# Kernel tuning notes

Measured on AMD Instinct MI355X. Metric: run time of the kernel, lower is better.

## Reference

```python
import jax, jax.numpy as jnp
import numpy as np

DIM_IN, DIM_OUT, DIM_CTX = 128, 256, 259
B, N, S_CTX = 32, 2048, 1
BN_EPS = 1e-5


def setup_inputs() -> dict:
    key = jax.random.key(0)
    ks = jax.random.split(key, 12)
    s = 0.02
    return {
        "ctx": jax.random.normal(ks[0], (B, S_CTX, DIM_CTX), jnp.float32),
        "x": jax.random.normal(ks[1], (B, N, DIM_IN), jnp.float32),
        "W_layer": jax.random.normal(ks[2], (DIM_OUT, DIM_IN), jnp.float32) * s,
        "b_layer": jax.random.normal(ks[3], (DIM_OUT,), jnp.float32) * s,
        "W_hbias": jax.random.normal(ks[4], (DIM_OUT, DIM_CTX), jnp.float32) * s,
        "W_gate": jax.random.normal(ks[5], (DIM_OUT, DIM_CTX), jnp.float32) * s,
        "b_gate": jax.random.normal(ks[6], (DIM_OUT,), jnp.float32) * s,
        "W_k": jax.random.normal(ks[7], (DIM_OUT, DIM_CTX - 3), jnp.float32) * s,
        "W_v": jax.random.normal(ks[8], (DIM_OUT, DIM_CTX - 3), jnp.float32) * s,
        "W_tc": jax.random.normal(ks[9], (DIM_OUT, DIM_OUT), jnp.float32) * s,
        "b_tc": jax.random.normal(ks[10], (DIM_OUT,), jnp.float32) * s,
        "bn_gamma": jnp.ones((N,), jnp.float32),
        "bn_beta": jnp.zeros((N,), jnp.float32),
    }


def reference(ctx, x, W_layer, b_layer, W_hbias, W_gate, b_gate, W_k, W_v, W_tc, b_tc, bn_gamma, bn_beta):
    # FiLM gate / bias from context: [B, 1, dim_out]
    gate = jax.nn.sigmoid(jnp.einsum('bsc,oc->bso', ctx, W_gate) + b_gate)
    bias = jnp.einsum('bsc,oc->bso', ctx, W_hbias)

    # main linear: [B, N, dim_out]
    x1 = jnp.einsum('bni,oi->bno', x, W_layer) + b_layer

    # channel attention from shape context (drop last 3 ctx dims)
    shape = ctx[:, :, : ctx.shape[2] - 3]                      # [B, S, C-3]
    shape_k = jnp.einsum('bsc,oc->bos', shape, W_k)            # [B, dim_out, S]
    shape_v = jnp.einsum('bsc,oc->bso', shape, W_v)            # [B, S, dim_out]
    energy = jnp.einsum('bos,bse->boe', shape_k, shape_v)      # [B, dim_out, dim_out]
    attention = jax.nn.softmax(energy, axis=-1)
    attention = attention / (1e-9 + attention.sum(axis=1, keepdims=True))

    # channel mixing: [B, N, dim_out]
    x_r = jnp.einsum('bno,boe->bne', x1, attention)

    # trans_conv + BatchNorm1d(N) (train-mode batch stats over dims (0, 2)) + ReLU
    t = jnp.einsum('bno,eo->bne', x1 - x_r, W_tc) + b_tc       # [B, N, dim_out]
    mean = t.mean(axis=(0, 2), keepdims=True)                  # per point-channel
    var = t.var(axis=(0, 2), keepdims=True)                    # biased variance
    t = (t - mean) * jax.lax.rsqrt(var + BN_EPS)
    t = t * bn_gamma[None, :, None] + bn_beta[None, :, None]
    x_r = jax.nn.relu(t)

    xo = x1 + x_r
    return xo * gate + bias
```

## Files before the change

kernel.cpp:

```cpp
#include <hip/hip_runtime.h>
#include <hip/hip_bf16.h>

#define BB   32
#define NN   2048
#define DIN  128
#define DOUT 256
#define DCTX 259

#define OFF_AB   0u
#define OFF_WMB  16777216u
#define OFF_WLB  17301504u
#define OFF_WLTB 17317888u
#define OFF_WTCB 17334272u
#define OFF_G    17367040u
#define OFF_HB   17375232u
#define OFF_TB   17383424u
#define OFF_P1   17655296u
#define OFF_P2   17720832u

typedef short bf16x8 __attribute__((ext_vector_type(8)));
typedef float f32x4  __attribute__((ext_vector_type(4)));

static __device__ inline unsigned short f2bf(float f) {
    __hip_bfloat16 h = __float2bfloat16(f);
    return *(unsigned short*)&h;
}
static __device__ inline float bf2f(unsigned short u) {
    unsigned v = ((unsigned)u) << 16;
    float f;
    __builtin_memcpy(&f, &v, 4);
    return f;
}

__global__ void kXW(const float* __restrict__ Wl, const float* __restrict__ Wtc,
                    float* __restrict__ ws) {
    unsigned bb = blockIdx.x, t = threadIdx.x;
    if (bb < 8u) {
        unsigned base = bb * 8192u;
        unsigned short* dst = (unsigned short*)(ws + OFF_WTCB);
#pragma unroll
        for (int j = 0; j < 32; j++) {
            unsigned i = base + (unsigned)j * 256u + t;
            dst[i] = f2bf(Wtc[i]);
        }
    } else if (bb == 8u) {
        unsigned short* dst = (unsigned short*)(ws + OFF_WLTB);
        for (unsigned idx = t; idx < 32768u; idx += 256u) {
            unsigned i = idx >> 8, o = idx & 255u;
            dst[idx] = f2bf(Wl[o * 128u + i]);
        }
    } else {
        unsigned short* dst = (unsigned short*)(ws + OFF_WLB);
        for (unsigned idx = t; idx < 32768u; idx += 256u) dst[idx] = f2bf(Wl[idx]);
    }
}

__global__ __launch_bounds__(1024) void kP(const float* __restrict__ ctx,
                                           const float* __restrict__ bg,
                                           const float* __restrict__ Wk,
                                           const float* __restrict__ Wv,
                                           const float* __restrict__ Wg,
                                           const float* __restrict__ Whb,
                                           float* __restrict__ ws) {
    const int b = blockIdx.x, t = threadIdx.x;
    const int o = t & 255, q = t >> 8;
    __shared__ __align__(16) float cs[260];
    __shared__ __align__(16) float ks[256], vs[256], rms[256], ris[256];
    __shared__ float pm[1024], ps[1024];
    for (int i = t; i < DCTX; i += 1024) cs[i] = ctx[b * DCTX + i];
    __syncthreads();

    {
        const float* Wm; int C;
        if (q == 0)      { Wm = Wk;  C = 256; }
        else if (q == 1) { Wm = Wv;  C = 256; }
        else if (q == 2) { Wm = Wg;  C = DCTX; }
        else             { Wm = Whb; C = DCTX; }
        const float* wr = Wm + (size_t)o * C;
        float s = 0.f;
#pragma unroll 16
        for (int c = 0; c < 256; c++) s += wr[c] * cs[c];
        if (C == DCTX) s += wr[256] * cs[256] + wr[257] * cs[257] + wr[258] * cs[258];
        if (q == 0)      ks[o] = s;
        else if (q == 1) vs[o] = s;
        else if (q == 2) ws[OFF_G + b * DOUT + o] = 1.f / (1.f + __expf(-(s + bg[o])));
        else             ws[OFF_HB + b * DOUT + o] = s;
    }
    __syncthreads();

    const float ko = ks[o];
    const float4* vs4 = (const float4*)vs;
    float pmax = -1e30f;
#pragma unroll 4
    for (int j = q * 16; j < q * 16 + 16; j++) {
        float4 v = vs4[j];
        pmax = fmaxf(pmax, fmaxf(fmaxf(ko * v.x, ko * v.y), fmaxf(ko * v.z, ko * v.w)));
    }
    pm[q * 256 + o] = pmax;
    __syncthreads();
    float m = fmaxf(fmaxf(pm[o], pm[256 + o]), fmaxf(pm[512 + o], pm[768 + o]));
    float psum = 0.f;
#pragma unroll 4
    for (int j = q * 16; j < q * 16 + 16; j++) {
        float4 v = vs4[j];
        psum += __expf(ko * v.x - m) + __expf(ko * v.y - m)
              + __expf(ko * v.z - m) + __expf(ko * v.w - m);
    }
    ps[q * 256 + o] = psum;
    __syncthreads();
    float ri = 1.f / (ps[o] + ps[256 + o] + ps[512 + o] + ps[768 + o]);
    if (q == 0) { rms[o] = m; ris[o] = ri; }
    __syncthreads();

    const float ve = vs[o];
    float cp = 0.f;
#pragma unroll 4
    for (int o2 = q * 64; o2 < q * 64 + 64; o2++)
        cp += __expf(ks[o2] * ve - rms[o2]) * ris[o2];
    pm[q * 256 + o] = cp;
    __syncthreads();
    float ci = 1.f / (1e-9f + pm[o] + pm[256 + o] + pm[512 + o] + pm[768 + o]);
    unsigned short* Ab = (unsigned short*)(ws + OFF_AB) + (size_t)b * 65536u;
#pragma unroll 4
    for (int o2 = q * 64; o2 < q * 64 + 64; o2++) {
        float a = __expf(ks[o2] * ve - rms[o2]) * ris[o2] * ci;
        Ab[o2 * 256 + o] = f2bf(a);
    }
}

__global__ __launch_bounds__(512) void k45(const float* __restrict__ bl,
                                           const float* __restrict__ btc,
                                           float* __restrict__ ws) {
    const int t = threadIdx.x, wid = t >> 6, l = t & 63;
    const int b = blockIdx.y, et = blockIdx.x;
    const int lrow = l & 15, lk = l >> 4;
    __shared__ unsigned short Mt[64 * 256];
    const unsigned short* Wtcb = (const unsigned short*)(ws + OFF_WTCB);

    {
        const unsigned short* Ab = (const unsigned short*)(ws + OFF_AB) + (size_t)b * 65536u;
        const int w_r = wid >> 2, w_c = wid & 3;
        const int rbase = et * 64 + w_r * 32;
        const int colbase = w_c * 64;
        f32x4 acc[2][4];
#pragma unroll
        for (int i = 0; i < 2; i++)
#pragma unroll
            for (int c = 0; c < 4; c++) acc[i][c] = (f32x4){0.f, 0.f, 0.f, 0.f};
        const unsigned short* ar0 = Wtcb + (rbase + lrow) * 256;
#pragma unroll
        for (int kk = 0; kk < 8; kk++) {
            int ko = kk * 32 + lk * 8;
            bf16x8 a0 = *(const bf16x8*)(ar0 + ko);
            bf16x8 a1 = *(const bf16x8*)(ar0 + 16 * 256 + ko);
            bf16x8 bfr[4];
#pragma unroll
            for (int c = 0; c < 4; c++)
                bfr[c] = *(const bf16x8*)(Ab + (colbase + c * 16 + lrow) * 256 + ko);
#pragma unroll
            for (int c = 0; c < 4; c++) {
                acc[0][c] = __builtin_amdgcn_mfma_f32_16x16x32_bf16(a0, bfr[c], acc[0][c], 0, 0, 0);
                acc[1][c] = __builtin_amdgcn_mfma_f32_16x16x32_bf16(a1, bfr[c], acc[1][c], 0, 0, 0);
            }
        }
#pragma unroll
        for (int t2 = 0; t2 < 2; t2++)
#pragma unroll
            for (int c = 0; c < 4; c++)
#pragma unroll
                for (int r = 0; r < 4; r++) {
                    int grow = rbase + t2 * 16 + lk * 4 + r;
                    int col = colbase + c * 16 + lrow;
                    float idv = bf2f(Wtcb[grow * 256 + col]);
                    int rl = grow - et * 64;
                    Mt[rl * 256 + (col ^ ((rl & 7) << 3))] = f2bf(idv - acc[t2][c][r]);
                }
    }
    __syncthreads();
    {
        const unsigned short* Wltb = (const unsigned short*)(ws + OFF_WLTB);
        const int w_r = wid >> 2, w_c = wid & 3;
        const int rl0 = w_r * 32;
        const int colb = w_c * 32;
        f32x4 acc[2][2];
#pragma unroll
        for (int i = 0; i < 2; i++)
#pragma unroll
            for (int c = 0; c < 2; c++) acc[i][c] = (f32x4){0.f, 0.f, 0.f, 0.f};
        const int arow0 = rl0 + lrow, arow1 = rl0 + 16 + lrow;
        const int asw0 = (arow0 & 7) << 3, asw1 = (arow1 & 7) << 3;
#pragma unroll
        for (int kk = 0; kk < 8; kk++) {
            int ko = kk * 32 + lk * 8;
            bf16x8 a0 = *(const bf16x8*)(Mt + arow0 * 256 + (ko ^ asw0));
            bf16x8 a1 = *(const bf16x8*)(Mt + arow1 * 256 + (ko ^ asw1));
            bf16x8 bfr[2];
#pragma unroll
            for (int c = 0; c < 2; c++)
                bfr[c] = *(const bf16x8*)(Wltb + (colb + c * 16 + lrow) * 256 + ko);
#pragma unroll
            for (int c = 0; c < 2; c++) {
                acc[0][c] = __builtin_amdgcn_mfma_f32_16x16x32_bf16(a0, bfr[c], acc[0][c], 0, 0, 0);
                acc[1][c] = __builtin_amdgcn_mfma_f32_16x16x32_bf16(a1, bfr[c], acc[1][c], 0, 0, 0);
            }
        }
        unsigned short* WMBp = (unsigned short*)(ws + OFF_WMB) + (size_t)b * 32768u;
#pragma unroll
        for (int t2 = 0; t2 < 2; t2++)
#pragma unroll
            for (int c = 0; c < 2; c++)
#pragma unroll
                for (int r = 0; r < 4; r++) {
                    int row = et * 64 + rl0 + t2 * 16 + lk * 4 + r;
                    int col = colb + c * 16 + lrow;
                    WMBp[row * 128 + col] = f2bf(acc[t2][c][r]);
                }
    }
    if (t < 64) {
        const int rl = t;
        const int sw = (rl & 7) << 3;
        float s = 0.f;
#pragma unroll 4
        for (int j = 0; j < 32; j++) {
            bf16x8 ch = *(const bf16x8*)(Mt + rl * 256 + ((j * 8) ^ sw));
#pragma unroll
            for (int u = 0; u < 8; u++) s += bl[j * 8 + u] * bf2f((unsigned short)ch[u]);
        }
        ws[OFF_TB + b * DOUT + et * 64 + rl] = s + btc[et * 64 + rl];
    }
}

#define LDP 136

__global__ __launch_bounds__(256) void kS(const float* __restrict__ x,
                                          float* __restrict__ ws) {
    const int t = threadIdx.x;
    const int wid = t >> 6, l = t & 63;
    const int b = blockIdx.x, nt = blockIdx.y;
    const int n0 = nt * 64;
    const int lrow = l & 15, lk = l >> 4;
    __shared__ unsigned short xs[64 * LDP];
    __shared__ float sp1[4][64], sp2[4][64];

    const float4* xg = (const float4*)(x + (size_t)(b * NN + n0) * DIN);
#pragma unroll
    for (int it = 0; it < 8; it++) {
        int idx = it * 256 + t;
        int row = idx >> 5, kq = idx & 31;
        float4 v = xg[idx];
        ushort4 u;
        u.x = f2bf(v.x); u.y = f2bf(v.y); u.z = f2bf(v.z); u.w = f2bf(v.w);
        *(ushort4*)(xs + row * LDP + kq * 4) = u;
    }
    __syncthreads();

    const int colbase = wid * 64;
    f32x4 acc[4][4];
#pragma unroll
    for (int rt = 0; rt < 4; rt++)
#pragma unroll
        for (int ct = 0; ct < 4; ct++) acc[rt][ct] = (f32x4){0.f, 0.f, 0.f, 0.f};
    {
        const unsigned short* wb = (const unsigned short*)(ws + OFF_WMB) + (size_t)b * 32768u;
#pragma unroll
        for (int kk = 0; kk < 4; kk++) {
            int ko = kk * 32 + lk * 8;
            bf16x8 a[4];
#pragma unroll
            for (int rt = 0; rt < 4; rt++)
                a[rt] = *(const bf16x8*)(xs + (rt * 16 + lrow) * LDP + ko);
            bf16x8 bf[4];
#pragma unroll
            for (int ct = 0; ct < 4; ct++)
                bf[ct] = *(const bf16x8*)(wb + (size_t)(colbase + ct * 16 + lrow) * DIN + ko);
#pragma unroll
            for (int rt = 0; rt < 4; rt++)
#pragma unroll
                for (int ct = 0; ct < 4; ct++)
                    acc[rt][ct] = __builtin_amdgcn_mfma_f32_16x16x32_bf16(a[rt], bf[ct], acc[rt][ct], 0, 0, 0);
        }
#pragma unroll
        for (int ct = 0; ct < 4; ct++) {
            float bv = ws[OFF_TB + b * DOUT + colbase + ct * 16 + lrow];
#pragma unroll
            for (int rt = 0; rt < 4; rt++)
#pragma unroll
                for (int r = 0; r < 4; r++) acc[rt][ct][r] += bv;
        }
    }

    float s1[4][4], s2[4][4];
#pragma unroll
    for (int rt = 0; rt < 4; rt++)
#pragma unroll
        for (int r = 0; r < 4; r++) { s1[rt][r] = 0.f; s2[rt][r] = 0.f; }
#pragma unroll
    for (int rt = 0; rt < 4; rt++)
#pragma unroll
        for (int ct = 0; ct < 4; ct++)
#pragma unroll
            for (int r = 0; r < 4; r++) {
                float v = acc[rt][ct][r];
                s1[rt][r] += v; s2[rt][r] += v * v;
            }
#pragma unroll
    for (int off = 1; off < 16; off <<= 1) {
#pragma unroll
        for (int rt = 0; rt < 4; rt++)
#pragma unroll
            for (int r = 0; r < 4; r++) {
                s1[rt][r] += __shfl_xor(s1[rt][r], off, 64);
                s2[rt][r] += __shfl_xor(s2[rt][r], off, 64);
            }
    }
    if (lrow == 0) {
#pragma unroll
        for (int rt = 0; rt < 4; rt++)
#pragma unroll
            for (int r = 0; r < 4; r++) {
                int nidx = rt * 16 + lk * 4 + r;
                sp1[wid][nidx] = s1[rt][r];
                sp2[wid][nidx] = s2[rt][r];
            }
    }
    __syncthreads();
    if (t < 64) {
        float S1 = sp1[0][t] + sp1[1][t] + sp1[2][t] + sp1[3][t];
        float S2 = sp2[0][t] + sp2[1][t] + sp2[2][t] + sp2[3][t];
        ws[OFF_P1 + (size_t)b * NN + n0 + t] = S1;
        ws[OFF_P2 + (size_t)b * NN + n0 + t] = S2;
    }
}

__global__ __launch_bounds__(256, 2) void kF(const float* __restrict__ x,
                                             const float* __restrict__ bl,
                                             const float* __restrict__ gamma,
                                             const float* __restrict__ beta,
                                             float* __restrict__ out,
                                             float* __restrict__ ws) {
    const int t = threadIdx.x;
    const int wid = t >> 6, l = t & 63;
    const int b = blockIdx.x;
    const int nt = blockIdx.y;
    const int n0 = nt * 64;
    const int lrow = l & 15, lk = l >> 4;
    __shared__ unsigned short xs[64 * LDP];
    __shared__ float scs[64], shs[64];

    const float4* xg = (const float4*)(x + (size_t)(b * NN + n0) * DIN);
    float4 xv[8];
#pragma unroll
    for (int it = 0; it < 8; it++) xv[it] = xg[it * 256 + t];

    if (t < 64) {
        float S1 = 0.f, S2 = 0.f;
#pragma unroll 8
        for (int b2 = 0; b2 < BB; b2++) {
            S1 += ws[OFF_P1 + (size_t)b2 * NN + n0 + t];
            S2 += ws[OFF_P2 + (size_t)b2 * NN + n0 + t];
        }
        float mean = S1 * (1.f / 8192.f);
        float var  = S2 * (1.f / 8192.f) - mean * mean;
        float sc = gamma[n0 + t] * rsqrtf(fmaxf(var, 0.f) + 1e-5f);
        scs[t] = sc;
        shs[t] = beta[n0 + t] - mean * sc;
    }
#pragma unroll
    for (int it = 0; it < 8; it++) {
        int idx = it * 256 + t;
        int row = idx >> 5, kq = idx & 31;
        ushort4 u;
        u.x = f2bf(xv[it].x); u.y = f2bf(xv[it].y); u.z = f2bf(xv[it].z); u.w = f2bf(xv[it].w);
        *(ushort4*)(xs + row * LDP + kq * 4) = u;
    }
    __syncthreads();

    const int colbase = wid * 64;

    f32x4 acc[4][4], acc0[4][4];
#pragma unroll
    for (int rt = 0; rt < 4; rt++)
#pragma unroll
        for (int ct = 0; ct < 4; ct++) {
            acc[rt][ct]  = (f32x4){0.f, 0.f, 0.f, 0.f};
            acc0[rt][ct] = (f32x4){0.f, 0.f, 0.f, 0.f};
        }
    {
        const unsigned short* wbM = (const unsigned short*)(ws + OFF_WMB) + (size_t)b * 32768u;
        const unsigned short* wbL = (const unsigned short*)(ws + OFF_WLB);
#pragma unroll
        for (int kk = 0; kk < 4; kk++) {
            int ko = kk * 32 + lk * 8;
            bf16x8 a[4];
#pragma unroll
            for (int rt = 0; rt < 4; rt++)
                a[rt] = *(const bf16x8*)(xs + (rt * 16 + lrow) * LDP + ko);
            bf16x8 bf[4];
#pragma unroll
            for (int ct = 0; ct < 4; ct++)
                bf[ct] = *(const bf16x8*)(wbM + (size_t)(colbase + ct * 16 + lrow) * DIN + ko);
#pragma unroll
            for (int rt = 0; rt < 4; rt++)
#pragma unroll
                for (int ct = 0; ct < 4; ct++)
                    acc[rt][ct] = __builtin_amdgcn_mfma_f32_16x16x32_bf16(a[rt], bf[ct], acc[rt][ct], 0, 0, 0);
#pragma unroll
            for (int ct = 0; ct < 4; ct++)
                bf[ct] = *(const bf16x8*)(wbL + (size_t)(colbase + ct * 16 + lrow) * DIN + ko);
#pragma unroll
            for (int rt = 0; rt < 4; rt++)
#pragma unroll
                for (int ct = 0; ct < 4; ct++)
                    acc0[rt][ct] = __builtin_amdgcn_mfma_f32_16x16x32_bf16(a[rt], bf[ct], acc0[rt][ct], 0, 0, 0);
        }
#pragma unroll
        for (int ct = 0; ct < 4; ct++) {
            float bvM = ws[OFF_TB + b * DOUT + colbase + ct * 16 + lrow];
            float bvL = bl[colbase + ct * 16 + lrow];
#pragma unroll
            for (int rt = 0; rt < 4; rt++)
#pragma unroll
                for (int r = 0; r < 4; r++) {
                    acc[rt][ct][r]  += bvM;
                    acc0[rt][ct][r] += bvL;
                }
        }
    }

    float gv[4], hbv[4];
#pragma unroll
    for (int ct = 0; ct < 4; ct++) {
        int o = colbase + ct * 16 + lrow;
        gv[ct]  = ws[OFF_G  + b * DOUT + o];
        hbv[ct] = ws[OFF_HB + b * DOUT + o];
    }
#pragma unroll
    for (int rt = 0; rt < 4; rt++)
#pragma unroll
        for (int r = 0; r < 4; r++) {
            int nidx = rt * 16 + lk * 4 + r;
            float sc = scs[nidx], sh = shs[nidx];
            int n = n0 + nidx;
#pragma unroll
            for (int ct = 0; ct < 4; ct++) {
                int o = colbase + ct * 16 + lrow;
                float rv = fmaxf(acc[rt][ct][r] * sc + sh, 0.f);
                out[(size_t)((b * NN + n) * DOUT) + o] = (acc0[rt][ct][r] + rv) * gv[ct] + hbv[ct];
            }
        }
}

extern "C" void kernel_launch(void* const* d_in, const int* in_sizes, int n_in,
                              void* d_out, int out_size, void* d_ws, size_t ws_size,
                              hipStream_t stream) {
    const float* ctx   = (const float*)d_in[0];
    const float* x     = (const float*)d_in[1];
    const float* Wl    = (const float*)d_in[2];
    const float* bl    = (const float*)d_in[3];
    const float* Whb   = (const float*)d_in[4];
    const float* Wg    = (const float*)d_in[5];
    const float* bg    = (const float*)d_in[6];
    const float* Wk    = (const float*)d_in[7];
    const float* Wv    = (const float*)d_in[8];
    const float* Wtc   = (const float*)d_in[9];
    const float* btc   = (const float*)d_in[10];
    const float* gamma = (const float*)d_in[11];
    const float* beta  = (const float*)d_in[12];
    float* out = (float*)d_out;
    float* ws  = (float*)d_ws;

    kXW <<<10, 256, 0, stream>>>(Wl, Wtc, ws);
    kP  <<<BB, 1024, 0, stream>>>(ctx, bg, Wk, Wv, Wg, Whb, ws);
    k45 <<<dim3(4, BB), 512, 0, stream>>>(bl, btc, ws);
    kS  <<<dim3(BB, 32), 256, 0, stream>>>(x, ws);
    kF  <<<dim3(BB, 32), 256, 0, stream>>>(x, bl, gamma, beta, out, ws);
}
```

Measured before the change: 237.2 us.

## Batch context projections across all batches in the weight-conversion kernel

The per-batch context projections (k, v, gate, hbias) move out of kP, where each of 32 blocks re-read all four weight matrices uncoalesced. They now run in 64 extra blocks of the weight-conversion kernel, each loading a 16-row weight tile plus all contexts into shared memory and computing two batches per thread. kP then only reads k/v from the workspace. kF splits the BN partial-sum reduction across all four waves instead of one, and its launch-bounds occupancy hint is dropped.

```diff
diff --git a/kernel.cpp b/kernel.cpp
--- a/kernel.cpp
+++ b/kernel.cpp
@@ -17,6 +17,8 @@
 #define OFF_TB   17383424u
 #define OFF_P1   17655296u
 #define OFF_P2   17720832u
+#define OFF_KS   17786368u
+#define OFF_VS   17794560u
 
 typedef short bf16x8 __attribute__((ext_vector_type(8)));
 typedef float f32x4  __attribute__((ext_vector_type(4)));
@@ -32,9 +34,19 @@
     return f;
 }
 
-__global__ void kXW(const float* __restrict__ Wl, const float* __restrict__ Wtc,
-                    float* __restrict__ ws) {
-    unsigned bb = blockIdx.x, t = threadIdx.x;
+__global__ __launch_bounds__(256) void kW(const float* __restrict__ Wl,
+                                          const float* __restrict__ Wtc,
+                                          const float* __restrict__ Wk,
+                                          const float* __restrict__ Wv,
+                                          const float* __restrict__ Wg,
+                                          const float* __restrict__ Whb,
+                                          const float* __restrict__ ctx,
+                                          const float* __restrict__ bg,
+                                          float* __restrict__ ws) {
+    const unsigned bb = blockIdx.x, t = threadIdx.x;
+    __shared__ float ctxs[32][260];
+    __shared__ float wt[16][260];
+
     if (bb < 8u) {
         unsigned base = bb * 8192u;
         unsigned short* dst = (unsigned short*)(ws + OFF_WTCB);
@@ -43,49 +55,71 @@
             unsigned i = base + (unsigned)j * 256u + t;
             dst[i] = f2bf(Wtc[i]);
         }
+        return;
     } else if (bb == 8u) {
         unsigned short* dst = (unsigned short*)(ws + OFF_WLTB);
         for (unsigned idx = t; idx < 32768u; idx += 256u) {
             unsigned i = idx >> 8, o = idx & 255u;
             dst[idx] = f2bf(Wl[o * 128u + i]);
         }
-    } else {
+        return;
+    } else if (bb == 9u) {
         unsigned short* dst = (unsigned short*)(ws + OFF_WLB);
         for (unsigned idx = t; idx < 32768u; idx += 256u) dst[idx] = f2bf(Wl[idx]);
-    }
-}
-
-__global__ __launch_bounds__(1024) void kP(const float* __restrict__ ctx,
-                                           const float* __restrict__ bg,
-                                           const float* __restrict__ Wk,
-                                           const float* __restrict__ Wv,
-                                           const float* __restrict__ Wg,
-                                           const float* __restrict__ Whb,
-                                           float* __restrict__ ws) {
+        return;
+    }
+
+    const int j = bb - 10;
+    const int m = j >> 4;
+    const int o0 = (j & 15) * 16;
+    const float* Wm; int C;
+    if (m == 0)      { Wm = Wk;  C = 256; }
+    else if (m == 1) { Wm = Wv;  C = 256; }
+    else if (m == 2) { Wm = Wg;  C = DCTX; }
+    else             { Wm = Whb; C = DCTX; }
+
+    for (int i = t; i < 32 * 260; i += 256) {
+        int b2 = i / 260, c = i - b2 * 260;
+        ctxs[b2][c] = (c < DCTX) ? ctx[b2 * DCTX + c] : 0.f;
+    }
+    for (int i = t; i < 16 * C; i += 256) {
+        int r = i / C, c = i - r * C;
+        wt[r][c] = Wm[(size_t)(o0 + r) * C + c];
+    }
+    __syncthreads();
+
+    const int ol = t & 15, b2 = t >> 4;
+    float s0 = 0.f, s1 = 0.f;
+#pragma unroll 8
+    for (int c = 0; c < C; c++) {
+        float w = wt[ol][c];
+        s0 += w * ctxs[b2][c];
+        s1 += w * ctxs[b2 + 16][c];
+    }
+    const int o = o0 + ol;
+    if (m == 0) {
+        ws[OFF_KS + b2 * DOUT + o] = s0;
+        ws[OFF_KS + (b2 + 16) * DOUT + o] = s1;
+    } else if (m == 1) {
+        ws[OFF_VS + b2 * DOUT + o] = s0;
+        ws[OFF_VS + (b2 + 16) * DOUT + o] = s1;
+    } else if (m == 2) {
+        float bgo = bg[o];
+        ws[OFF_G + b2 * DOUT + o] = 1.f / (1.f + __expf(-(s0 + bgo)));
+        ws[OFF_G + (b2 + 16) * DOUT + o] = 1.f / (1.f + __expf(-(s1 + bgo)));
+    } else {
+        ws[OFF_HB + b2 * DOUT + o] = s0;
+        ws[OFF_HB + (b2 + 16) * DOUT + o] = s1;
+    }
+}
+
+__global__ __launch_bounds__(1024) void kP(float* __restrict__ ws) {
     const int b = blockIdx.x, t = threadIdx.x;
     const int o = t & 255, q = t >> 8;
-    __shared__ __align__(16) float cs[260];
     __shared__ __align__(16) float ks[256], vs[256], rms[256], ris[256];
     __shared__ float pm[1024], ps[1024];
-    for (int i = t; i < DCTX; i += 1024) cs[i] = ctx[b * DCTX + i];
-    __syncthreads();
-
-    {
-        const float* Wm; int C;
-        if (q == 0)      { Wm = Wk;  C = 256; }
-        else if (q == 1) { Wm = Wv;  C = 256; }
-        else if (q == 2) { Wm = Wg;  C = DCTX; }
-        else             { Wm = Whb; C = DCTX; }
-        const float* wr = Wm + (size_t)o * C;
-        float s = 0.f;
-#pragma unroll 16
-        for (int c = 0; c < 256; c++) s += wr[c] * cs[c];
-        if (C == DCTX) s += wr[256] * cs[256] + wr[257] * cs[257] + wr[258] * cs[258];
-        if (q == 0)      ks[o] = s;
-        else if (q == 1) vs[o] = s;
-        else if (q == 2) ws[OFF_G + b * DOUT + o] = 1.f / (1.f + __expf(-(s + bg[o])));
-        else             ws[OFF_HB + b * DOUT + o] = s;
-    }
+    if (t < 256)            ks[t] = ws[OFF_KS + b * DOUT + t];
+    else if (t < 512)       vs[t - 256] = ws[OFF_VS + b * DOUT + (t - 256)];
     __syncthreads();
 
     const float ko = ks[o];
@@ -332,12 +366,12 @@
     }
 }
 
-__global__ __launch_bounds__(256, 2) void kF(const float* __restrict__ x,
-                                             const float* __restrict__ bl,
-                                             const float* __restrict__ gamma,
-                                             const float* __restrict__ beta,
-                                             float* __restrict__ out,
-                                             float* __restrict__ ws) {
+__global__ __launch_bounds__(256) void kF(const float* __restrict__ x,
+                                          const float* __restrict__ bl,
+                                          const float* __restrict__ gamma,
+                                          const float* __restrict__ beta,
+                                          float* __restrict__ out,
+                                          float* __restrict__ ws) {
     const int t = threadIdx.x;
     const int wid = t >> 6, l = t & 63;
     const int b = blockIdx.x;
@@ -345,6 +379,7 @@
     const int n0 = nt * 64;
     const int lrow = l & 15, lk = l >> 4;
     __shared__ unsigned short xs[64 * LDP];
+    __shared__ float sq1[4][64], sq2[4][64];
     __shared__ float scs[64], shs[64];
 
     const float4* xg = (const float4*)(x + (size_t)(b * NN + n0) * DIN);
@@ -352,13 +387,20 @@
 #pragma unroll
     for (int it = 0; it < 8; it++) xv[it] = xg[it * 256 + t];
 
+    {
+        int n = t & 63, g = t >> 6;
+        float S1 = 0.f, S2 = 0.f;
+#pragma unroll
+        for (int b2 = g * 8; b2 < g * 8 + 8; b2++) {
+            S1 += ws[OFF_P1 + (size_t)b2 * NN + n0 + n];
+            S2 += ws[OFF_P2 + (size_t)b2 * NN + n0 + n];
+        }
+        sq1[g][n] = S1; sq2[g][n] = S2;
+    }
+    __syncthreads();
     if (t < 64) {
-        float S1 = 0.f, S2 = 0.f;
-#pragma unroll 8
-        for (int b2 = 0; b2 < BB; b2++) {
-            S1 += ws[OFF_P1 + (size_t)b2 * NN + n0 + t];
-            S2 += ws[OFF_P2 + (size_t)b2 * NN + n0 + t];
-        }
+        float S1 = sq1[0][t] + sq1[1][t] + sq1[2][t] + sq1[3][t];
+        float S2 = sq2[0][t] + sq2[1][t] + sq2[2][t] + sq2[3][t];
         float mean = S1 * (1.f / 8192.f);
         float var  = S2 * (1.f / 8192.f) - mean * mean;
         float sc = gamma[n0 + t] * rsqrtf(fmaxf(var, 0.f) + 1e-5f);
@@ -469,8 +511,8 @@
     float* out = (float*)d_out;
     float* ws  = (float*)d_ws;
 
-    kXW <<<10, 256, 0, stream>>>(Wl, Wtc, ws);
-    kP  <<<BB, 1024, 0, stream>>>(ctx, bg, Wk, Wv, Wg, Whb, ws);
+    kW  <<<74, 256, 0, stream>>>(Wl, Wtc, Wk, Wv, Wg, Whb, ctx, bg, ws);
+    kP  <<<BB, 1024, 0, stream>>>(ws);
     k45 <<<dim3(4, BB), 512, 0, stream>>>(bl, btc, ws);
     kS  <<<dim3(BB, 32), 256, 0, stream>>>(x, ws);
     kF  <<<dim3(BB, 32), 256, 0, stream>>>(x, bl, gamma, beta, out, ws);
```

Result: faster. 208.7 us (-12.0%).
